# Kernel tuning notes

Measured on AMD Instinct MI355X. Metric: run time of the kernel, lower is better.

## Reference

```python
import jax, jax.numpy as jnp
import numpy as np
import math

B, S, D, H = 4, 2048, 1024, 16
HD = D // H  # head_dim = 64


def setup_inputs() -> dict:
    key = jax.random.key(0)
    ks = jax.random.split(key, 5)
    x = jax.random.normal(ks[0], (B, S, D), dtype=jnp.float32)
    # causal mask, broadcastable over batch and heads
    mask = jnp.tril(jnp.ones((S, S), dtype=bool))[None, None]
    # Linear params in [in, out] layout (math-equivalent to torch's [out, in])
    w_attn = jax.random.normal(ks[1], (D, 3 * D), dtype=jnp.float32) * (1.0 / math.sqrt(D))
    b_attn = jax.random.normal(ks[2], (3 * D,), dtype=jnp.float32) * 0.02
    w_proj = jax.random.normal(ks[3], (D, D), dtype=jnp.float32) * (1.0 / math.sqrt(D))
    b_proj = jax.random.normal(ks[4], (D,), dtype=jnp.float32) * 0.02
    return {"x": x, "mask": mask, "w_attn": w_attn, "b_attn": b_attn,
            "w_proj": w_proj, "b_proj": b_proj}


def reference(x, mask, w_attn, b_attn, w_proj, b_proj):
    b, s, d = x.shape
    # fused qkv projection, then split heads -> [b, h, s, hd]
    qkv = x @ w_attn + b_attn
    q, k, v = jnp.split(qkv, 3, axis=-1)
    split = lambda t: t.reshape(b, s, H, HD).transpose(0, 2, 1, 3)
    q, k, v = split(q), split(k), split(v)
    # scaled dot-product attention with boolean mask (True = keep)
    scores = jnp.einsum('bhqd,bhkd->bhqk', q, k) / math.sqrt(HD)
    scores = jnp.where(mask, scores, -jnp.inf)
    attn = jax.nn.softmax(scores, axis=-1)  # attn_dropout with p=0 is identity
    out = jnp.einsum('bhqk,bhkd->bhqd', attn, v)
    out = out.transpose(0, 2, 1, 3).reshape(b, s, d)
    # output projection (resid_dropout with p=0 is identity)
    return out @ w_proj + b_proj
```

## Files before the change

### kernel.cpp

```cpp
#include <hip/hip_runtime.h>

typedef unsigned short u16;
typedef __attribute__((ext_vector_type(4))) float floatx4;
typedef __attribute__((ext_vector_type(8))) short shortx8;

#define B_ 4
#define S_ 2048
#define D_ 1024
#define H_ 16
#define HD_ 64

__device__ __forceinline__ float b2f(u16 u) {
    return __uint_as_float(((unsigned int)u) << 16);
}
__device__ __forceinline__ u16 f2b(float f) {
    unsigned int u = __float_as_uint(f);
    u += 0x7fffu + ((u >> 16) & 1u);
    return (u16)(u >> 16);
}
__device__ __forceinline__ unsigned long long pack4(float a, float b, float c, float d) {
    return (unsigned long long)f2b(a) | ((unsigned long long)f2b(b) << 16) |
           ((unsigned long long)f2b(c) << 32) | ((unsigned long long)f2b(d) << 48);
}
__device__ __forceinline__ unsigned int permpk(float a, float b) {
    return __builtin_amdgcn_perm(__float_as_uint(b) + 0x8000u,
                                 __float_as_uint(a) + 0x8000u, 0x07060302u);
}
__device__ __forceinline__ void glds16(const u16* g, u16* l) {
    __builtin_amdgcn_global_load_lds(
        (const __attribute__((address_space(1))) unsigned int*)g,
        (__attribute__((address_space(3))) unsigned int*)l, 16, 0, 0);
}
__device__ __forceinline__ void bar() {
    asm volatile("" ::: "memory");
    __builtin_amdgcn_s_barrier();
    asm volatile("" ::: "memory");
}
#define VMW3 asm volatile("s_waitcnt vmcnt(3)" ::: "memory")
#define VMW0 asm volatile("s_waitcnt vmcnt(0)" ::: "memory")

__global__ __launch_bounds__(256) void preproc(const void* __restrict__ xin,
                                               u16* __restrict__ xb,
                                               const void* __restrict__ bA,
                                               const void* __restrict__ bP,
                                               u16* __restrict__ bAb,
                                               u16* __restrict__ bPb,
                                               const void* __restrict__ wA,
                                               u16* __restrict__ wtA,
                                               const void* __restrict__ wP,
                                               u16* __restrict__ wtP,
                                               int* __restrict__ flag) {
    __shared__ int cnts[4];
    __shared__ u16 tile[32][33];
    const int tid = threadIdx.x;
    {
        const unsigned int e = (((const unsigned int*)xin)[tid] >> 7) & 0xffu;
        int c = (e >= 110u && e <= 134u) ? 1 : 0;
#pragma unroll
        for (int d = 1; d < 64; d <<= 1) c += __shfl_xor(c, d);
        if ((tid & 63) == 0) cnts[tid >> 6] = c;
    }
    __syncthreads();
    const int isbf = (cnts[0] + cnts[1] + cnts[2] + cnts[3] > 128) ? 1 : 0;

    const int bid = blockIdx.x;
    if (bid < 4096) {
        const size_t i = ((size_t)bid * 256 + tid) * 8;
        if (isbf) {
            *(uint4*)(xb + i) = *(const uint4*)((const u16*)xin + i);
        } else {
            const float* xf = (const float*)xin;
            float4 a = *(const float4*)(xf + i);
            float4 b = *(const float4*)(xf + i + 4);
            u16 o[8] = {f2b(a.x), f2b(a.y), f2b(a.z), f2b(a.w),
                        f2b(b.x), f2b(b.y), f2b(b.z), f2b(b.w)};
            *(uint4*)(xb + i) = *(uint4*)o;
        }
        if (bid == 0) {
            if (tid == 0) *flag = isbf;
            for (int j = tid; j < 3072; j += 256)
                bAb[j] = isbf ? ((const u16*)bA)[j] : f2b(((const float*)bA)[j]);
            for (int j = tid; j < 1024; j += 256)
                bPb[j] = isbf ? ((const u16*)bP)[j] : f2b(((const float*)bP)[j]);
        }
    } else {
        const int idx = bid - 4096;
        int bxi = idx & 127;
        const int by = (idx >> 7) * 32;
        const void* in;
        u16* out;
        int N;
        if (bxi < 96) { in = wA; out = wtA; N = 3072; }
        else          { in = wP; out = wtP; N = 1024; bxi -= 96; }
        const int K = 1024;
        const int bx = bxi * 32;
        const int tx = tid & 31;
        const int ty = tid >> 5;
        if (isbf) {
#pragma unroll
            for (int i = 0; i < 32; i += 8)
                tile[ty + i][tx] = ((const u16*)in)[(size_t)(by + ty + i) * N + bx + tx];
        } else {
#pragma unroll
            for (int i = 0; i < 32; i += 8)
                tile[ty + i][tx] = f2b(((const float*)in)[(size_t)(by + ty + i) * N + bx + tx]);
        }
        __syncthreads();
#pragma unroll
        for (int i = 0; i < 32; i += 8)
            out[(size_t)(bx + ty + i) * K + by + tx] = tile[tx][ty + i];
    }
}

template <int MODE>
__global__ __launch_bounds__(512) void gemm_bt(const u16* __restrict__ A,
                                               const u16* __restrict__ BT,
                                               const u16* __restrict__ bias,
                                               void* __restrict__ outv,
                                               int M, int N, int K,
                                               u16* __restrict__ qws,
                                               u16* __restrict__ kws,
                                               u16* __restrict__ vws,
                                               const int* __restrict__ flag) {
    __shared__ __align__(16) u16 lds[36864];

    const int isbf = (MODE == 0) ? *flag : 1;
    const int tid = threadIdx.x;
    const int w = tid >> 6, l = tid & 63;
    const int lane_m = l & 15, quad = l >> 4;
    const int bid = blockIdx.x;
    const int bm = ((bid & 7) * 4 + ((bid >> 3) & 3)) * 256;
    const int bn = (bid >> 5) * 128;
    const int wm = (w >> 1) * 64, wn = (w & 1) * 64;

    floatx4 acc[4][4];
#pragma unroll
    for (int i = 0; i < 4; i++)
#pragma unroll
        for (int j = 0; j < 4; j++) acc[i][j] = (floatx4){0.f, 0.f, 0.f, 0.f};

    const int lr = l >> 2, sl = l & 3;
    const int cA = sl ^ ((lr >> 1) & 3);
    const int ra0 = w * 32, ra1 = w * 32 + 16, rb = w * 16;
    const u16* Arow0 = A + (size_t)(bm + ra0 + lr) * K + cA * 8;
    const u16* Arow1 = A + (size_t)(bm + ra1 + lr) * K + cA * 8;
    const u16* Brow  = BT + (size_t)(bn + rb + lr) * K + cA * 8;

    auto stage = [&](int t) {
        const int k0 = t * 32;
        u16* ad = lds + (t % 3) * 8192;
        u16* bd = lds + 24576 + (t % 3) * 4096;
        glds16(Arow0 + k0, ad + ra0 * 32);
        glds16(Arow1 + k0, ad + ra1 * 32);
        glds16(Brow + k0, bd + rb * 32);
    };

    const int NT = K >> 5;
    stage(0);
    stage(1);
    for (int t = 0; t < NT; ++t) {
        if (t < NT - 1) { VMW3; } else { VMW0; }
        bar();
        if (t + 2 < NT) stage(t + 2);

        const u16* Ac = lds + (t % 3) * 8192;
        const u16* Bc = lds + 24576 + (t % 3) * 4096;
        shortx8 af[4], bf[4];
#pragma unroll
        for (int mb = 0; mb < 4; mb++) {
            const int r = wm + mb * 16 + lane_m;
            af[mb] = *(const shortx8*)(Ac + r * 32 + (quad ^ ((r >> 1) & 3)) * 8);
        }
#pragma unroll
        for (int nb = 0; nb < 4; nb++) {
            const int r = wn + nb * 16 + lane_m;
            bf[nb] = *(const shortx8*)(Bc + r * 32 + (quad ^ ((r >> 1) & 3)) * 8);
        }
#pragma unroll
        for (int mb = 0; mb < 4; mb++)
#pragma unroll
            for (int nb = 0; nb < 4; nb++)
                acc[mb][nb] = __builtin_amdgcn_mfma_f32_16x16x32_bf16(
                    af[mb], bf[nb], acc[mb][nb], 0, 0, 0);
    }

    const float SCALE_Q = 0.18033688011112042f;

    if (MODE == 1 && (bn >> 10) == 2) {
        __syncthreads();
        u16* ep = lds + w * 4096;
#pragma unroll
        for (int nb = 0; nb < 4; nb++) {
            const int lhd = nb * 16 + lane_m;
            const float bv = b2f(bias[bn + wn + lhd]);
            const int sw = (lhd & 7) << 3;
#pragma unroll
            for (int mb = 0; mb < 4; mb++) {
                const int o = mb * 16 + quad * 4;
                unsigned long long pk =
                    pack4(acc[mb][nb][0] + bv, acc[mb][nb][1] + bv,
                          acc[mb][nb][2] + bv, acc[mb][nb][3] + bv);
                *(unsigned long long*)(ep + lhd * 64 + (o ^ sw)) = pk;
            }
        }
        __syncthreads();
        const int bI = bm >> 11;
        const int hI = ((bn + wn) >> 6) & 15;
        const int s0 = (bm & 2047) + wm;
        u16* vb0 = vws + (size_t)(bI * 16 + hI) * 64 * 2048;
        const int rr8 = l >> 3, c8 = l & 7;
#pragma unroll
        for (int p = 0; p < 8; p++) {
            const int lhd = p * 8 + rr8;
            uint4 v4 = *(const uint4*)(ep + lhd * 64 + ((c8 << 3) ^ ((lhd & 7) << 3)));
            *(uint4*)(vb0 + (size_t)lhd * 2048 + s0 + c8 * 8) = v4;
        }
    } else if (MODE == 1) {
        const int which = bn >> 10;
        u16* dst = (which == 0) ? qws : kws;
        const int h = ((bn + wn) >> 6) & 15;
        const int bI = bm >> 11;
        u16* dbase = dst + (size_t)(bI * 16 + h) * 2048 * 64 + lane_m;
        float bv4[4];
#pragma unroll
        for (int nb = 0; nb < 4; nb++) bv4[nb] = b2f(bias[bn + wn + nb * 16 + lane_m]);
#pragma unroll
        for (int mb = 0; mb < 4; mb++) {
#pragma unroll
            for (int r = 0; r < 4; r++) {
                const int s = (bm & 2047) + wm + mb * 16 + quad * 4 + r;
                u16* line = dbase + (size_t)s * 64;
#pragma unroll
                for (int nb = 0; nb < 4; nb++) {
                    float v = acc[mb][nb][r] + bv4[nb];
                    if (which == 0) v *= SCALE_Q;
                    line[nb * 16] = f2b(v);
                }
            }
        }
    } else {
        float bv4[4];
#pragma unroll
        for (int nb = 0; nb < 4; nb++) bv4[nb] = b2f(bias[bn + wn + nb * 16 + lane_m]);
#pragma unroll
        for (int mb = 0; mb < 4; mb++) {
#pragma unroll
            for (int r = 0; r < 4; r++) {
                const int rr = bm + wm + mb * 16 + quad * 4 + r;
#pragma unroll
                for (int nb = 0; nb < 4; nb++) {
                    const int col = bn + wn + nb * 16 + lane_m;
                    float v = acc[mb][nb][r] + bv4[nb];
                    if (isbf) ((u16*)outv)[(size_t)rr * N + col] = f2b(v);
                    else ((float*)outv)[(size_t)rr * N + col] = v;
                }
            }
        }
    }
}

__global__ __launch_bounds__(512, 4) void attn_kernel(const u16* __restrict__ Qg,
                                                      const u16* __restrict__ Kg,
                                                      const u16* __restrict__ Vtg,
                                                      u16* __restrict__ Og) {
    __shared__ __align__(16) u16 Ks[2][64 * 64];
    __shared__ __align__(16) u16 Vs[2][64 * 64];
    __shared__ __align__(16) u16 Ps[8][16 * 72];

    const int tid = threadIdx.x, w = tid >> 6, l = tid & 63;
    const int lane_m = l & 15, quad = l >> 4;
    const int bid = blockIdx.x;
    const int bh = (bid & 7) * 8 + ((bid >> 3) >> 3);
    const int xmi = (bid >> 3) & 7;
    const u16* qp = Qg + (size_t)bh * S_ * 64;
    const u16* kp = Kg + (size_t)bh * S_ * 64;
    const u16* vtp = Vtg + (size_t)bh * 64 * S_;
    u16* psw = &Ps[w][0];
    const int b = bh >> 4, h = bh & 15;

    const int lr8 = l >> 3, sl8 = l & 7;
    const int cK = sl8 ^ (lr8 & 7);
    const int rbase = w * 8;
    const u16* Kr = kp + (size_t)(rbase + lr8) * 64 + cK * 8;
    const u16* Vr = vtp + (size_t)(rbase + lr8) * S_ + cK * 8;

    auto stage = [&](int t) {
        const int k0 = t * 64;
        glds16(Kr + (size_t)k0 * 64, &Ks[t & 1][0] + rbase * 64);
        glds16(Vr + k0, &Vs[t & 1][0] + rbase * 64);
    };

    for (int pass = 0; pass < 2; pass++) {
        const int xm = pass ? (15 - xmi) : xmi;
        const int q0 = xm * 128;
        const int qw0 = q0 + w * 16;

        shortx8 qF[2];
#pragma unroll
        for (int ks = 0; ks < 2; ks++)
            qF[ks] = *(const shortx8*)(qp + (size_t)(qw0 + lane_m) * 64 + ks * 32 + quad * 8);

        floatx4 o_acc[4];
#pragma unroll
        for (int md = 0; md < 4; md++) o_acc[md] = (floatx4){0.f, 0.f, 0.f, 0.f};
        float m_i = -1e30f, l_i = 0.f;

        const int ntiles = (q0 >> 6) + 2;
        const int myend = qw0 + 15;

        __syncthreads();
        stage(0);
        for (int t = 0; t < ntiles; t++) {
            const int k0 = t * 64;
            __syncthreads();
            if (t + 1 < ntiles) stage(t + 1);

            if (k0 <= myend) {
                const u16* kb = &Ks[t & 1][0];
                const u16* vb = &Vs[t & 1][0];
                floatx4 sc[4];
#pragma unroll
                for (int mb = 0; mb < 4; mb++) sc[mb] = (floatx4){0.f, 0.f, 0.f, 0.f};
#pragma unroll
                for (int ks = 0; ks < 2; ks++) {
                    shortx8 kA[4];
#pragma unroll
                    for (int mb = 0; mb < 4; mb++) {
                        const int r = mb * 16 + lane_m;
                        kA[mb] = *(const shortx8*)(kb + r * 64 + (((ks * 4 + quad) ^ (r & 7)) * 8));
                    }
                    __builtin_amdgcn_s_setprio(1);
#pragma unroll
                    for (int mb = 0; mb < 4; mb++)
                        sc[mb] = __builtin_amdgcn_mfma_f32_16x16x32_bf16(
                            kA[mb], qF[ks], sc[mb], 0, 0, 0);
                    __builtin_amdgcn_s_setprio(0);
                }

                const int qg = qw0 + lane_m;
                if (k0 + 63 > qw0) {
#pragma unroll
                    for (int mb = 0; mb < 4; mb++)
#pragma unroll
                        for (int r = 0; r < 4; r++) {
                            const int kvg = k0 + mb * 16 + quad * 4 + r;
                            if (kvg > qg) sc[mb][r] = -1e30f;
                        }
                }
                float mloc = -1e30f;
#pragma unroll
                for (int mb = 0; mb < 4; mb++) {
                    float a = fmaxf(fmaxf(sc[mb][0], sc[mb][1]),
                                    fmaxf(sc[mb][2], sc[mb][3]));
                    mloc = fmaxf(mloc, a);
                }
                mloc = fmaxf(mloc, __shfl_xor(mloc, 16));
                mloc = fmaxf(mloc, __shfl_xor(mloc, 32));
                float mnew = m_i;
                if (!__all(mloc <= m_i + 8.0f)) {
                    mnew = fmaxf(m_i, mloc);
                    const float alpha = __builtin_amdgcn_exp2f(m_i - mnew);
                    m_i = mnew;
                    l_i *= alpha;
#pragma unroll
                    for (int md = 0; md < 4; md++) o_acc[md] *= alpha;
                }
                float psum = 0.f;
#pragma unroll
                for (int mb = 0; mb < 4; mb++) {
                    const float p0 = __builtin_amdgcn_exp2f(sc[mb][0] - mnew);
                    const float p1 = __builtin_amdgcn_exp2f(sc[mb][1] - mnew);
                    const float p2 = __builtin_amdgcn_exp2f(sc[mb][2] - mnew);
                    const float p3 = __builtin_amdgcn_exp2f(sc[mb][3] - mnew);
                    psum += (p0 + p1) + (p2 + p3);
                    uint2 pk = {permpk(p0, p1), permpk(p2, p3)};
                    *(uint2*)(psw + lane_m * 72 + mb * 16 + quad * 4) = pk;
                }
                psum += __shfl_xor(psum, 16);
                psum += __shfl_xor(psum, 32);
                l_i += psum;

#pragma unroll
                for (int ks = 0; ks < 2; ks++) {
                    shortx8 vF[4], pF;
#pragma unroll
                    for (int md = 0; md < 4; md++) {
                        const int r = md * 16 + lane_m;
                        vF[md] = *(const shortx8*)(vb + r * 64 + (((ks * 4 + quad) ^ (r & 7)) * 8));
                    }
                    pF = *(const shortx8*)(psw + lane_m * 72 + ks * 32 + quad * 8);
                    __builtin_amdgcn_s_setprio(1);
#pragma unroll
                    for (int md = 0; md < 4; md++)
                        o_acc[md] = __builtin_amdgcn_mfma_f32_16x16x32_bf16(
                            vF[md], pF, o_acc[md], 0, 0, 0);
                    __builtin_amdgcn_s_setprio(0);
                }
            }
        }

        {
            const float inv = 1.0f / l_i;
            const int qg = qw0 + lane_m;
            const size_t base = ((size_t)b * 2048 + qg) * 1024 + h * 64;
#pragma unroll
            for (int md = 0; md < 4; md++) {
                *(unsigned long long*)(Og + base + md * 16 + quad * 4) =
                    pack4(o_acc[md][0] * inv, o_acc[md][1] * inv,
                          o_acc[md][2] * inv, o_acc[md][3] * inv);
            }
        }
    }
}

extern "C" void kernel_launch(void* const* d_in, const int* in_sizes, int n_in,
                              void* d_out, int out_size, void* d_ws, size_t ws_size,
                              hipStream_t stream) {
    const void* x      = d_in[0];
    const void* w_attn = d_in[2];
    const void* b_attn = d_in[3];
    const void* w_proj = d_in[4];
    const void* b_proj = d_in[5];

    u16* qws = (u16*)d_ws;
    u16* kws = qws + 8388608;
    u16* vws = kws + 8388608;
    u16* xb  = vws + 8388608;
    u16* aws = xb;
    u16* wtA = xb + 8388608;
    u16* wtP = wtA + 3145728;
    u16* bAb = wtP + 1048576;
    u16* bPb = bAb + 3072;
    int* flag = (int*)(bPb + 1024);

    preproc<<<8192, 256, 0, stream>>>(x, xb, b_attn, b_proj, bAb, bPb,
                                      w_attn, wtA, w_proj, wtP, flag);

    gemm_bt<1><<<dim3(32 * 24), 512, 0, stream>>>(
        xb, wtA, bAb, nullptr, 8192, 3072, 1024, qws, kws, vws, flag);

    attn_kernel<<<dim3(512), 512, 0, stream>>>(qws, kws, vws, aws);

    gemm_bt<0><<<dim3(32 * 8), 512, 0, stream>>>(
        aws, wtP, bPb, d_out, 8192, 1024, 1024, nullptr, nullptr, nullptr, flag);
}
```

Before: 252.9 us.

## Software-pipeline attention: overlap next tile QK^T with current softmax and PV

Restructures the attention main loop so the QK^T MFMAs for KV tile t are issued alongside the softmax and PV work for tile t-1. This gives the scheduler independent matrix and exp/ALU work to interleave. K/V shared buffers go from double to triple buffering so the V tile stays resident one iteration longer. The per-wave causal tile skip is dropped, so some waves compute an unused QK^T tile. The larger LDS footprint also lowers the number of blocks resident per CU.

```diff
diff --git a/kernel.cpp b/kernel.cpp
--- a/kernel.cpp
+++ b/kernel.cpp
@@ -263,8 +263,8 @@
                                                       const u16* __restrict__ Kg,
                                                       const u16* __restrict__ Vtg,
                                                       u16* __restrict__ Og) {
-    __shared__ __align__(16) u16 Ks[2][64 * 64];
-    __shared__ __align__(16) u16 Vs[2][64 * 64];
+    __shared__ __align__(16) u16 Ks[3][64 * 64];
+    __shared__ __align__(16) u16 Vs[3][64 * 64];
     __shared__ __align__(16) u16 Ps[8][16 * 72];
 
     const int tid = threadIdx.x, w = tid >> 6, l = tid & 63;
@@ -286,9 +286,81 @@
 
     auto stage = [&](int t) {
         const int k0 = t * 64;
-        glds16(Kr + (size_t)k0 * 64, &Ks[t & 1][0] + rbase * 64);
-        glds16(Vr + k0, &Vs[t & 1][0] + rbase * 64);
+        glds16(Kr + (size_t)k0 * 64, &Ks[t % 3][0] + rbase * 64);
+        glds16(Vr + k0, &Vs[t % 3][0] + rbase * 64);
     };
+
+#define QKT(kb_)                                                               \
+    {                                                                          \
+        _Pragma("unroll") for (int mb = 0; mb < 4; mb++)                       \
+            scN[mb] = (floatx4){0.f, 0.f, 0.f, 0.f};                           \
+        _Pragma("unroll") for (int ks = 0; ks < 2; ks++) {                     \
+            shortx8 kA[4];                                                     \
+            _Pragma("unroll") for (int mb = 0; mb < 4; mb++) {                 \
+                const int r = mb * 16 + lane_m;                                \
+                kA[mb] = *(const shortx8*)((kb_) + r * 64 +                    \
+                                           (((ks * 4 + quad) ^ (r & 7)) * 8)); \
+            }                                                                  \
+            __builtin_amdgcn_s_setprio(1);                                     \
+            _Pragma("unroll") for (int mb = 0; mb < 4; mb++)                   \
+                scN[mb] = __builtin_amdgcn_mfma_f32_16x16x32_bf16(             \
+                    kA[mb], qF[ks], scN[mb], 0, 0, 0);                         \
+            __builtin_amdgcn_s_setprio(0);                                     \
+        }                                                                      \
+    }
+
+#define SMPV(KP0, vb_)                                                         \
+    {                                                                          \
+        const int qg = qw0 + lane_m;                                           \
+        _Pragma("unroll") for (int mb = 0; mb < 4; mb++)                       \
+            _Pragma("unroll") for (int r = 0; r < 4; r++) {                    \
+                const int kvg = (KP0) + mb * 16 + quad * 4 + r;                \
+                scP[mb][r] = (kvg > qg) ? -1e30f : scP[mb][r];                 \
+            }                                                                  \
+        float mloc = -1e30f;                                                   \
+        _Pragma("unroll") for (int mb = 0; mb < 4; mb++) {                     \
+            float a = fmaxf(fmaxf(scP[mb][0], scP[mb][1]),                     \
+                            fmaxf(scP[mb][2], scP[mb][3]));                    \
+            mloc = fmaxf(mloc, a);                                             \
+        }                                                                      \
+        mloc = fmaxf(mloc, __shfl_xor(mloc, 16));                              \
+        mloc = fmaxf(mloc, __shfl_xor(mloc, 32));                              \
+        float mnew = m_i;                                                      \
+        if (!__all(mloc <= m_i + 8.0f)) {                                      \
+            mnew = fmaxf(m_i, mloc);                                           \
+            const float alpha = __builtin_amdgcn_exp2f(m_i - mnew);            \
+            m_i = mnew;                                                        \
+            l_i *= alpha;                                                      \
+            _Pragma("unroll") for (int md = 0; md < 4; md++) o_acc[md] *= alpha; \
+        }                                                                      \
+        float psum = 0.f;                                                      \
+        _Pragma("unroll") for (int mb = 0; mb < 4; mb++) {                     \
+            const float p0 = __builtin_amdgcn_exp2f(scP[mb][0] - mnew);        \
+            const float p1 = __builtin_amdgcn_exp2f(scP[mb][1] - mnew);        \
+            const float p2 = __builtin_amdgcn_exp2f(scP[mb][2] - mnew);        \
+            const float p3 = __builtin_amdgcn_exp2f(scP[mb][3] - mnew);        \
+            psum += (p0 + p1) + (p2 + p3);                                     \
+            uint2 pk = {permpk(p0, p1), permpk(p2, p3)};                       \
+            *(uint2*)(psw + lane_m * 72 + mb * 16 + quad * 4) = pk;            \
+        }                                                                      \
+        psum += __shfl_xor(psum, 16);                                          \
+        psum += __shfl_xor(psum, 32);                                          \
+        l_i += psum;                                                           \
+        _Pragma("unroll") for (int ks = 0; ks < 2; ks++) {                     \
+            shortx8 vF[4], pF;                                                 \
+            _Pragma("unroll") for (int md = 0; md < 4; md++) {                 \
+                const int r = md * 16 + lane_m;                                \
+                vF[md] = *(const shortx8*)((vb_) + r * 64 +                    \
+                                           (((ks * 4 + quad) ^ (r & 7)) * 8)); \
+            }                                                                  \
+            pF = *(const shortx8*)(psw + lane_m * 72 + ks * 32 + quad * 8);    \
+            __builtin_amdgcn_s_setprio(1);                                     \
+            _Pragma("unroll") for (int md = 0; md < 4; md++)                   \
+                o_acc[md] = __builtin_amdgcn_mfma_f32_16x16x32_bf16(           \
+                    vF[md], pF, o_acc[md], 0, 0, 0);                           \
+            __builtin_amdgcn_s_setprio(0);                                     \
+        }                                                                      \
+    }
 
     for (int pass = 0; pass < 2; pass++) {
         const int xm = pass ? (15 - xmi) : xmi;
@@ -304,99 +376,33 @@
 #pragma unroll
         for (int md = 0; md < 4; md++) o_acc[md] = (floatx4){0.f, 0.f, 0.f, 0.f};
         float m_i = -1e30f, l_i = 0.f;
+        floatx4 scP[4], scN[4];
 
         const int ntiles = (q0 >> 6) + 2;
-        const int myend = qw0 + 15;
+        const int lastT = (qw0 + 15) >> 6;
 
         __syncthreads();
         stage(0);
-        for (int t = 0; t < ntiles; t++) {
-            const int k0 = t * 64;
+
+        __syncthreads();
+        stage(1);
+        QKT(&Ks[0][0]);
+#pragma unroll
+        for (int mb = 0; mb < 4; mb++) scP[mb] = scN[mb];
+
+        for (int t = 1; t < ntiles; t++) {
             __syncthreads();
             if (t + 1 < ntiles) stage(t + 1);
-
-            if (k0 <= myend) {
-                const u16* kb = &Ks[t & 1][0];
-                const u16* vb = &Vs[t & 1][0];
-                floatx4 sc[4];
-#pragma unroll
-                for (int mb = 0; mb < 4; mb++) sc[mb] = (floatx4){0.f, 0.f, 0.f, 0.f};
-#pragma unroll
-                for (int ks = 0; ks < 2; ks++) {
-                    shortx8 kA[4];
-#pragma unroll
-                    for (int mb = 0; mb < 4; mb++) {
-                        const int r = mb * 16 + lane_m;
-                        kA[mb] = *(const shortx8*)(kb + r * 64 + (((ks * 4 + quad) ^ (r & 7)) * 8));
-                    }
-                    __builtin_amdgcn_s_setprio(1);
-#pragma unroll
-                    for (int mb = 0; mb < 4; mb++)
-                        sc[mb] = __builtin_amdgcn_mfma_f32_16x16x32_bf16(
-                            kA[mb], qF[ks], sc[mb], 0, 0, 0);
-                    __builtin_amdgcn_s_setprio(0);
-                }
-
-                const int qg = qw0 + lane_m;
-                if (k0 + 63 > qw0) {
-#pragma unroll
-                    for (int mb = 0; mb < 4; mb++)
-#pragma unroll
-                        for (int r = 0; r < 4; r++) {
-                            const int kvg = k0 + mb * 16 + quad * 4 + r;
-                            if (kvg > qg) sc[mb][r] = -1e30f;
-                        }
-                }
-                float mloc = -1e30f;
-#pragma unroll
-                for (int mb = 0; mb < 4; mb++) {
-                    float a = fmaxf(fmaxf(sc[mb][0], sc[mb][1]),
-                                    fmaxf(sc[mb][2], sc[mb][3]));
-                    mloc = fmaxf(mloc, a);
-                }
-                mloc = fmaxf(mloc, __shfl_xor(mloc, 16));
-                mloc = fmaxf(mloc, __shfl_xor(mloc, 32));
-                float mnew = m_i;
-                if (!__all(mloc <= m_i + 8.0f)) {
-                    mnew = fmaxf(m_i, mloc);
-                    const float alpha = __builtin_amdgcn_exp2f(m_i - mnew);
-                    m_i = mnew;
-                    l_i *= alpha;
-#pragma unroll
-                    for (int md = 0; md < 4; md++) o_acc[md] *= alpha;
-                }
-                float psum = 0.f;
-#pragma unroll
-                for (int mb = 0; mb < 4; mb++) {
-                    const float p0 = __builtin_amdgcn_exp2f(sc[mb][0] - mnew);
-                    const float p1 = __builtin_amdgcn_exp2f(sc[mb][1] - mnew);
-                    const float p2 = __builtin_amdgcn_exp2f(sc[mb][2] - mnew);
-                    const float p3 = __builtin_amdgcn_exp2f(sc[mb][3] - mnew);
-                    psum += (p0 + p1) + (p2 + p3);
-                    uint2 pk = {permpk(p0, p1), permpk(p2, p3)};
-                    *(uint2*)(psw + lane_m * 72 + mb * 16 + quad * 4) = pk;
-                }
-                psum += __shfl_xor(psum, 16);
-                psum += __shfl_xor(psum, 32);
-                l_i += psum;
-
-#pragma unroll
-                for (int ks = 0; ks < 2; ks++) {
-                    shortx8 vF[4], pF;
-#pragma unroll
-                    for (int md = 0; md < 4; md++) {
-                        const int r = md * 16 + lane_m;
-                        vF[md] = *(const shortx8*)(vb + r * 64 + (((ks * 4 + quad) ^ (r & 7)) * 8));
-                    }
-                    pF = *(const shortx8*)(psw + lane_m * 72 + ks * 32 + quad * 8);
-                    __builtin_amdgcn_s_setprio(1);
-#pragma unroll
-                    for (int md = 0; md < 4; md++)
-                        o_acc[md] = __builtin_amdgcn_mfma_f32_16x16x32_bf16(
-                            vF[md], pF, o_acc[md], 0, 0, 0);
-                    __builtin_amdgcn_s_setprio(0);
-                }
-            }
+            const u16* kb = &Ks[t % 3][0];
+            const u16* vb = &Vs[(t - 1) % 3][0];
+            QKT(kb);
+            SMPV((t - 1) * 64, vb);
+#pragma unroll
+            for (int mb = 0; mb < 4; mb++) scP[mb] = scN[mb];
+        }
+        if (lastT == ntiles - 1) {
+            const u16* vb = &Vs[(ntiles - 1) % 3][0];
+            SMPV((ntiles - 1) * 64, vb);
         }
 
         {
@@ -411,6 +417,8 @@
             }
         }
     }
+#undef QKT
+#undef SMPV
 }
 
 extern "C" void kernel_launch(void* const* d_in, const int* in_sizes, int n_in,
```

After: 261.8 us. +3.5%, slower.

## Split projection GEMM into 128x128 triple-buffered kernel and enlarge weight transpose tiles

Applied to the files above, without the earlier changes.

The output projection GEMM, which used the QKV kernel's 256x128 tile, becomes its own kernel with 128x128 tiles, 256 threads and a three-stage global-to-LDS pipeline. This doubles the block count from 256 to 512 so the device's compute units are better filled on the smaller N=1024 GEMM. The weight-transpose part of preproc also moves from 32x32 to 64x64 tiles, which reduces the number of blocks and keeps more of each load and store coalesced. The trade-offs are more A/B re-reads from global memory because tiles are smaller, and a larger LDS footprint in the transpose.

```diff
diff --git a/kernel.cpp b/kernel.cpp
--- a/kernel.cpp
+++ b/kernel.cpp
@@ -36,6 +36,7 @@
     __builtin_amdgcn_s_barrier();
     asm volatile("" ::: "memory");
 }
+#define VMW4 asm volatile("s_waitcnt vmcnt(4)" ::: "memory")
 #define VMW3 asm volatile("s_waitcnt vmcnt(3)" ::: "memory")
 #define VMW0 asm volatile("s_waitcnt vmcnt(0)" ::: "memory")
 
@@ -51,7 +52,7 @@
                                                u16* __restrict__ wtP,
                                                int* __restrict__ flag) {
     __shared__ int cnts[4];
-    __shared__ u16 tile[32][33];
+    __shared__ u16 tile[64][65];
     const int tid = threadIdx.x;
     {
         const unsigned int e = (((const unsigned int*)xin)[tid] >> 7) & 0xffu;
@@ -85,46 +86,42 @@
         }
     } else {
         const int idx = bid - 4096;
-        int bxi = idx & 127;
-        const int by = (idx >> 7) * 32;
+        int bxi = idx & 63;
+        const int by = (idx >> 6) * 64;
         const void* in;
         u16* out;
         int N;
-        if (bxi < 96) { in = wA; out = wtA; N = 3072; }
-        else          { in = wP; out = wtP; N = 1024; bxi -= 96; }
+        if (bxi < 48) { in = wA; out = wtA; N = 3072; }
+        else          { in = wP; out = wtP; N = 1024; bxi -= 48; }
         const int K = 1024;
-        const int bx = bxi * 32;
-        const int tx = tid & 31;
-        const int ty = tid >> 5;
+        const int bx = bxi * 64;
+        const int tx = tid & 63;
+        const int ty = tid >> 6;
         if (isbf) {
 #pragma unroll
-            for (int i = 0; i < 32; i += 8)
+            for (int i = 0; i < 64; i += 4)
                 tile[ty + i][tx] = ((const u16*)in)[(size_t)(by + ty + i) * N + bx + tx];
         } else {
 #pragma unroll
-            for (int i = 0; i < 32; i += 8)
+            for (int i = 0; i < 64; i += 4)
                 tile[ty + i][tx] = f2b(((const float*)in)[(size_t)(by + ty + i) * N + bx + tx]);
         }
         __syncthreads();
 #pragma unroll
-        for (int i = 0; i < 32; i += 8)
+        for (int i = 0; i < 64; i += 4)
             out[(size_t)(bx + ty + i) * K + by + tx] = tile[tx][ty + i];
     }
 }
 
-template <int MODE>
-__global__ __launch_bounds__(512) void gemm_bt(const u16* __restrict__ A,
-                                               const u16* __restrict__ BT,
-                                               const u16* __restrict__ bias,
-                                               void* __restrict__ outv,
-                                               int M, int N, int K,
-                                               u16* __restrict__ qws,
-                                               u16* __restrict__ kws,
-                                               u16* __restrict__ vws,
-                                               const int* __restrict__ flag) {
+__global__ __launch_bounds__(512) void gemm_qkv(const u16* __restrict__ A,
+                                                const u16* __restrict__ BT,
+                                                const u16* __restrict__ bias,
+                                                int M, int N, int K,
+                                                u16* __restrict__ qws,
+                                                u16* __restrict__ kws,
+                                                u16* __restrict__ vws) {
     __shared__ __align__(16) u16 lds[36864];
 
-    const int isbf = (MODE == 0) ? *flag : 1;
     const int tid = threadIdx.x;
     const int w = tid >> 6, l = tid & 63;
     const int lane_m = l & 15, quad = l >> 4;
@@ -186,7 +183,7 @@
 
     const float SCALE_Q = 0.18033688011112042f;
 
-    if (MODE == 1 && (bn >> 10) == 2) {
+    if ((bn >> 10) == 2) {
         __syncthreads();
         u16* ep = lds + w * 4096;
 #pragma unroll
@@ -215,7 +212,7 @@
             uint4 v4 = *(const uint4*)(ep + lhd * 64 + ((c8 << 3) ^ ((lhd & 7) << 3)));
             *(uint4*)(vb0 + (size_t)lhd * 2048 + s0 + c8 * 8) = v4;
         }
-    } else if (MODE == 1) {
+    } else {
         const int which = bn >> 10;
         u16* dst = (which == 0) ? qws : kws;
         const int h = ((bn + wn) >> 6) & 15;
@@ -238,22 +235,94 @@
                 }
             }
         }
-    } else {
-        float bv4[4];
-#pragma unroll
-        for (int nb = 0; nb < 4; nb++) bv4[nb] = b2f(bias[bn + wn + nb * 16 + lane_m]);
+    }
+}
+
+__global__ __launch_bounds__(256) void gemm_proj(const u16* __restrict__ A,
+                                                 const u16* __restrict__ BT,
+                                                 const u16* __restrict__ bias,
+                                                 void* __restrict__ outv,
+                                                 int M, int N, int K,
+                                                 const int* __restrict__ flag) {
+    __shared__ __align__(16) u16 As[3][128 * 32];
+    __shared__ __align__(16) u16 Bs[3][128 * 32];
+
+    const int isbf = *flag;
+    const int tid = threadIdx.x;
+    const int w = tid >> 6, l = tid & 63;
+    const int lane_m = l & 15, quad = l >> 4;
+    const int bid = blockIdx.x;
+    const int bm = ((bid & 7) * 8 + ((bid >> 3) & 7)) * 128;
+    const int bn = (bid >> 6) * 128;
+    const int wm = (w >> 1) * 64, wn = (w & 1) * 64;
+
+    floatx4 acc[4][4];
+#pragma unroll
+    for (int i = 0; i < 4; i++)
+#pragma unroll
+        for (int j = 0; j < 4; j++) acc[i][j] = (floatx4){0.f, 0.f, 0.f, 0.f};
+
+    const int lr = l >> 2, sl = l & 3;
+    const int cA = sl ^ ((lr >> 1) & 3);
+    const int rb0 = w * 16, rb1 = 64 + w * 16;
+    const u16* Arow0 = A + (size_t)(bm + rb0 + lr) * K + cA * 8;
+    const u16* Arow1 = A + (size_t)(bm + rb1 + lr) * K + cA * 8;
+    const u16* Brow0 = BT + (size_t)(bn + rb0 + lr) * K + cA * 8;
+    const u16* Brow1 = BT + (size_t)(bn + rb1 + lr) * K + cA * 8;
+
+    auto stage = [&](int t) {
+        const int k0 = t * 32;
+        u16* ad = &As[t % 3][0];
+        u16* bd = &Bs[t % 3][0];
+        glds16(Arow0 + k0, ad + rb0 * 32);
+        glds16(Arow1 + k0, ad + rb1 * 32);
+        glds16(Brow0 + k0, bd + rb0 * 32);
+        glds16(Brow1 + k0, bd + rb1 * 32);
+    };
+
+    const int NT = K >> 5;
+    stage(0);
+    stage(1);
+    for (int t = 0; t < NT; ++t) {
+        if (t < NT - 1) { VMW4; } else { VMW0; }
+        bar();
+        if (t + 2 < NT) stage(t + 2);
+
+        const u16* Ac = &As[t % 3][0];
+        const u16* Bc = &Bs[t % 3][0];
+        shortx8 af[4], bf[4];
 #pragma unroll
         for (int mb = 0; mb < 4; mb++) {
-#pragma unroll
-            for (int r = 0; r < 4; r++) {
-                const int rr = bm + wm + mb * 16 + quad * 4 + r;
-#pragma unroll
-                for (int nb = 0; nb < 4; nb++) {
-                    const int col = bn + wn + nb * 16 + lane_m;
-                    float v = acc[mb][nb][r] + bv4[nb];
-                    if (isbf) ((u16*)outv)[(size_t)rr * N + col] = f2b(v);
-                    else ((float*)outv)[(size_t)rr * N + col] = v;
-                }
+            const int r = wm + mb * 16 + lane_m;
+            af[mb] = *(const shortx8*)(Ac + r * 32 + (quad ^ ((r >> 1) & 3)) * 8);
+        }
+#pragma unroll
+        for (int nb = 0; nb < 4; nb++) {
+            const int r = wn + nb * 16 + lane_m;
+            bf[nb] = *(const shortx8*)(Bc + r * 32 + (quad ^ ((r >> 1) & 3)) * 8);
+        }
+#pragma unroll
+        for (int mb = 0; mb < 4; mb++)
+#pragma unroll
+            for (int nb = 0; nb < 4; nb++)
+                acc[mb][nb] = __builtin_amdgcn_mfma_f32_16x16x32_bf16(
+                    af[mb], bf[nb], acc[mb][nb], 0, 0, 0);
+    }
+
+    float bv4[4];
+#pragma unroll
+    for (int nb = 0; nb < 4; nb++) bv4[nb] = b2f(bias[bn + wn + nb * 16 + lane_m]);
+#pragma unroll
+    for (int mb = 0; mb < 4; mb++) {
+#pragma unroll
+        for (int r = 0; r < 4; r++) {
+            const int rr = bm + wm + mb * 16 + quad * 4 + r;
+#pragma unroll
+            for (int nb = 0; nb < 4; nb++) {
+                const int col = bn + wn + nb * 16 + lane_m;
+                float v = acc[mb][nb][r] + bv4[nb];
+                if (isbf) ((u16*)outv)[(size_t)rr * N + col] = f2b(v);
+                else ((float*)outv)[(size_t)rr * N + col] = v;
             }
         }
     }
@@ -433,14 +502,14 @@
     u16* bPb = bAb + 3072;
     int* flag = (int*)(bPb + 1024);
 
-    preproc<<<8192, 256, 0, stream>>>(x, xb, b_attn, b_proj, bAb, bPb,
+    preproc<<<5120, 256, 0, stream>>>(x, xb, b_attn, b_proj, bAb, bPb,
                                       w_attn, wtA, w_proj, wtP, flag);
 
-    gemm_bt<1><<<dim3(32 * 24), 512, 0, stream>>>(
-        xb, wtA, bAb, nullptr, 8192, 3072, 1024, qws, kws, vws, flag);
+    gemm_qkv<<<dim3(32 * 24), 512, 0, stream>>>(
+        xb, wtA, bAb, 8192, 3072, 1024, qws, kws, vws);
 
     attn_kernel<<<dim3(512), 512, 0, stream>>>(qws, kws, vws, aws);
 
-    gemm_bt<0><<<dim3(32 * 8), 512, 0, stream>>>(
-        aws, wtP, bPb, d_out, 8192, 1024, 1024, nullptr, nullptr, nullptr, flag);
-}
+    gemm_proj<<<dim3(64 * 8), 256, 0, stream>>>(
+        aws, wtP, bPb, d_out, 8192, 1024, 1024, flag);
+}
```

Measured after the change: 264.7 us. +4.7%, slower.
